# Performance work log

Hardware: AMD Instinct MI355X
Metric: run time of the kernel (lower is better)

## Reference

```python
import jax, jax.numpy as jnp
import numpy as np

N_WIRES = 16
VAR_DEPTH = 2
BATCH = 16


def _param_sizes():
    sizes = []
    n = N_WIRES
    lay = 0
    while n > 1:
        sizes.append(4 * int(np.ceil(N_WIRES / 2 ** lay)) * VAR_DEPTH)
        n = (n + 1) // 2
        lay += 1
    return sizes  # [128, 64, 32, 16]


def _apply_1q(psi, gate, w):
    # psi: (B, 2, ..., 2); gate: (2,2) complex; wire w lives on axis w+1
    psi = jnp.moveaxis(psi, w + 1, -1)
    psi = jnp.einsum('...j,ij->...i', psi, gate)
    return jnp.moveaxis(psi, -1, w + 1)


def _rx(psi, th, w):
    c = jnp.cos(th / 2).astype(jnp.complex64)
    s = jnp.sin(th / 2).astype(jnp.complex64)
    gate = jnp.stack([jnp.stack([c, -1j * s]), jnp.stack([-1j * s, c])])
    return _apply_1q(psi, gate, w)


def _rz(psi, th, w):
    ph = jnp.exp(0.5j * th * jnp.array([-1.0, 1.0], jnp.float32)).astype(jnp.complex64)
    shape = [1] * psi.ndim
    shape[w + 1] = 2
    return psi * ph.reshape(shape)


def _rzz(psi, th, wa, wb):
    # diag(e^{-i t/2}, e^{i t/2}, e^{i t/2}, e^{-i t/2}) -> sign = -1 if bits equal else +1
    sgn = jnp.array([[-1.0, 1.0], [1.0, -1.0]], jnp.float32)
    ph = jnp.exp(0.5j * th * sgn).astype(jnp.complex64)  # symmetric, transpose-safe
    a, b = min(wa, wb) + 1, max(wa, wb) + 1
    shape = [1] * psi.ndim
    shape[a] = 2
    shape[b] = 2
    return psi * ph.reshape(shape)


def _cnot(psi, c, t):
    p0 = jax.lax.slice_in_dim(psi, 0, 1, axis=c + 1)
    p1 = jax.lax.slice_in_dim(psi, 1, 2, axis=c + 1)
    return jnp.concatenate([p0, jnp.flip(p1, axis=t + 1)], axis=c + 1)


def _conv_layer(psi, params, active):
    n = len(active)
    for d in range(VAR_DEPTH):
        for j in range(n):
            base = 4 * j + d * 4 * n
            psi = _rx(psi, params[base + 0], active[j])
            psi = _rz(psi, params[base + 1], active[j])
            psi = _rx(psi, params[base + 2], active[j])
        for bg in (0, 1):
            for j in range(bg, n, 2):
                jn = (j + 1) % n  # ring coupling (wraps last->first)
                base = 4 * j + d * 4 * n
                psi = _rzz(psi, params[base + 3], active[j], active[jn])
    return psi


def _pool(psi, active):
    for j in range(0, len(active), 2):
        if j + 1 < len(active):
            psi = _cnot(psi, active[j], active[j + 1])
    return psi, active[::2]


def _forward(psi, params_list):
    active = list(range(N_WIRES))
    for p in params_list:
        psi = _conv_layer(psi, p, active)
        if len(active) > 1:
            psi, active = _pool(psi, active)
    w = active[0]  # measure Z on the surviving wire (wire 0)
    prob = psi.real ** 2 + psi.imag ** 2
    axes = tuple(a for a in range(1, psi.ndim) if a != w + 1)
    p2 = prob.sum(axis=axes)  # (B, 2)
    return p2[:, 0] - p2[:, 1]


def setup_inputs() -> dict:
    key = jax.random.key(0)
    ks = jax.random.split(key, 8)
    dim = 2 ** N_WIRES
    x_re = jax.random.normal(ks[0], (BATCH, dim), dtype=jnp.float32)
    x_im = jax.random.normal(ks[1], (BATCH, dim), dtype=jnp.float32)
    nrm = jnp.sqrt(jnp.sum(x_re ** 2 + x_im ** 2, axis=1, keepdims=True))
    x_re = x_re / nrm
    x_im = x_im / nrm
    sizes = _param_sizes()
    two_pi = 2.0 * np.pi
    params = [jax.random.uniform(ks[2 + i], (sizes[i],), dtype=jnp.float32) * two_pi
              for i in range(len(sizes))]
    return {"x_re": x_re, "x_im": x_im,
            "params0": params[0], "params1": params[1],
            "params2": params[2], "params3": params[3]}


def reference(x_re, x_im, params0, params1, params2, params3):
    psi = (x_re + 1j * x_im).astype(jnp.complex64)
    psi = psi.reshape((BATCH,) + (2,) * N_WIRES)
    return _forward(psi, [params0, params1, params2, params3])
```

## Files before the change

### kernel.cpp

```cpp
#include <hip/hip_runtime.h>


#define DEV __device__ __forceinline__
#define TB(i) (tbl + (i)*8)

__device__ static const unsigned char G_CP[60] = {
  15,14,13,12,11,10,9,8,7,6,5,4,3,2,1,0,
  15,14,13,12,11,10,9,8,7,6,5,4,3,2,1,0,
  15,13,11,9,7,5,3,1,
  15,13,11,9,7,5,3,1,
  15,11,7,3,
  15,11,7,3,
  15,7,
  15,7
};
__device__ static const unsigned char G_CQ[60] = {
  14,13,12,11,10,9,8,7,6,5,4,3,2,1,0,15,
  14,13,12,11,10,9,8,7,6,5,4,3,2,1,0,15,
  13,11,9,7,5,3,1,15,
  13,11,9,7,5,3,1,15,
  11,7,3,15,
  11,7,3,15,
  7,15,
  7,15
};

DEV float2 F2(float x, float y){ float2 r; r.x = x; r.y = y; return r; }
DEV float2 cmulf(float2 a, float2 b){ return F2(a.x*b.x - a.y*b.y, a.x*b.y + a.y*b.x); }
DEV int swz(int j){ return j ^ ((j>>4)&15) ^ ((j>>6)&15); }

template<int B>
DEV void gate8(float2* a, const float* __restrict__ g){
  float u00r=g[0],u00i=g[1],u01r=g[2],u01i=g[3],u10r=g[4],u10i=g[5],u11r=g[6],u11i=g[7];
  #pragma unroll
  for (int m=0; m<4; m++){
    int i0 = ((m>>B)<<(B+1)) | (m & ((1<<B)-1));
    int i1 = i0 | (1<<B);
    float2 x0=a[i0], x1=a[i1];
    a[i0] = F2(u00r*x0.x - u00i*x0.y + u01r*x1.x - u01i*x1.y,
               u00r*x0.y + u00i*x0.x + u01r*x1.y + u01i*x1.x);
    a[i1] = F2(u10r*x0.x - u10i*x0.y + u11r*x1.x - u11i*x1.y,
               u10r*x0.y + u10i*x0.x + u11r*x1.y + u11i*x1.x);
  }
}

template<int CB,int TB>
DEV void cnot8(float2* a){
  #pragma unroll
  for (int r=0; r<8; r++){
    if ( ((r>>CB)&1)==1 && ((r>>TB)&1)==0 ){
      float2 tmp = a[r]; a[r] = a[r | (1<<TB)]; a[r | (1<<TB)] = tmp;
    }
  }
}

template<int C0,int N,unsigned M0,unsigned M1,unsigned M2>
DEV void diag8(float2* a, const float* __restrict__ tbl, unsigned Ib){
  const unsigned regmask = M0|M1|M2;
  float2 F0 = F2(1.f, 0.f);
  #pragma unroll
  for (int k=0; k<N; k++){
    const int p = G_CP[C0+k], q = G_CQ[C0+k];
    if ( !(((1u<<p)|(1u<<q)) & regmask) ){
      float c = tbl[480 + 2*(C0+k)], s = tbl[481 + 2*(C0+k)];
      unsigned x = ((Ib>>p) ^ (Ib>>q)) & 1u;
      F0 = cmulf(F0, F2(c, x ? s : -s));
    }
  }
  #pragma unroll
  for (int r=0; r<8; r++){
    unsigned Ir = Ib ^ ((r&1)?M0:0u) ^ ((r&2)?M1:0u) ^ ((r&4)?M2:0u);
    float2 ph = F0;
    #pragma unroll
    for (int k=0; k<N; k++){
      const int p = G_CP[C0+k], q = G_CQ[C0+k];
      if ( ((1u<<p)|(1u<<q)) & regmask ){
        float c = tbl[480 + 2*(C0+k)], s = tbl[481 + 2*(C0+k)];
        unsigned x = ((Ir>>p) ^ (Ir>>q)) & 1u;
        ph = cmulf(ph, F2(c, x ? s : -s));
      }
    }
    a[r] = cmulf(a[r], ph);
  }
}

__global__ void k_setup(const float* __restrict__ p0, const float* __restrict__ p1,
                        const float* __restrict__ p2, const float* __restrict__ p3,
                        float* __restrict__ tbl, float* __restrict__ out){
  int g = threadIdx.x;
  if (g < 16) out[g] = 0.f;
  if (g >= 60) return;
  int d, j, n; const float* P;
  if (g < 32)      { n=16; d=(g>>4)&1; j=g&15; P=p0; }
  else if (g < 48) { n=8;  d=(g>>3)&1; j=g&7;  P=p1; }
  else if (g < 56) { n=4;  d=(g>>2)&1; j=g&3;  P=p2; }
  else             { n=2;  d=(g>>1)&1; j=g&1;  P=p3; }
  int base = 4*j + 4*n*d;
  double th0 = P[base+0], th1 = P[base+1], th2 = P[base+2], th3 = P[base+3];
  double c0 = cos(th0*0.5), s0 = sin(th0*0.5);
  double ca = cos(th1*0.5), sa = sin(th1*0.5);
  double c2 = cos(th2*0.5), s2 = sin(th2*0.5);
  double B00r =  ca*c0, B00i = -sa*c0;
  double B01r = -sa*s0, B01i = -ca*s0;
  double B10r =  sa*s0, B10i = -ca*s0;
  double B11r =  ca*c0, B11i =  sa*c0;
  double U00r = c2*B00r + s2*B10i, U00i = c2*B00i - s2*B10r;
  double U01r = c2*B01r + s2*B11i, U01i = c2*B01i - s2*B11r;
  double U10r = s2*B00i + c2*B10r, U10i = -s2*B00r + c2*B10i;
  double U11r = s2*B01i + c2*B11r, U11i = -s2*B01r + c2*B11i;
  float* o = tbl + g*8;
  o[0]=(float)U00r; o[1]=(float)U00i; o[2]=(float)U01r; o[3]=(float)U01i;
  o[4]=(float)U10r; o[5]=(float)U10i; o[6]=(float)U11r; o[7]=(float)U11i;
  tbl[480 + 2*g] = (float)cos(th3*0.5);
  tbl[481 + 2*g] = (float)sin(th3*0.5);
}

__global__ __launch_bounds__(128) void k_pass1(const float* __restrict__ xre, const float* __restrict__ xim,
                                               const float* __restrict__ tbl, float2* __restrict__ st){
  const int t = threadIdx.x;
  const int batch = blockIdx.x >> 6, o = blockIdx.x & 63;
  const unsigned hi = ((unsigned)batch<<16) | ((unsigned)o<<10);
  __shared__ float2 lds[2][1024];
  float2 a[8];
  {
    unsigned base = hi | ((unsigned)t<<3);
    float4 r0 = *(const float4*)(xre+base), r1 = *(const float4*)(xre+base+4);
    float4 i0 = *(const float4*)(xim+base), i1 = *(const float4*)(xim+base+4);
    a[0]=F2(r0.x,i0.x); a[1]=F2(r0.y,i0.y); a[2]=F2(r0.z,i0.z); a[3]=F2(r0.w,i0.w);
    a[4]=F2(r1.x,i1.x); a[5]=F2(r1.y,i1.y); a[6]=F2(r1.z,i1.z); a[7]=F2(r1.w,i1.w);
  }
  gate8<0>(a, TB(15)); gate8<1>(a, TB(14)); gate8<2>(a, TB(13));
  #pragma unroll
  for (int r=0;r<8;r++) lds[0][swz(r | (t<<3))] = a[r];
  __syncthreads();
  #pragma unroll
  for (int r=0;r<8;r++) a[r] = lds[0][swz((t&7) | (r<<3) | ((t>>3)<<6))];
  gate8<0>(a, TB(12)); gate8<1>(a, TB(11)); gate8<2>(a, TB(10));
  #pragma unroll
  for (int r=0;r<8;r++) lds[1][swz((t&7) | (r<<3) | ((t>>3)<<6))] = a[r];
  __syncthreads();
  #pragma unroll
  for (int r=0;r<8;r++) a[r] = lds[1][swz((t&63) | (r<<6) | ((t>>6)<<9))];
  gate8<0>(a, TB(9)); gate8<1>(a, TB(8)); gate8<2>(a, TB(7));
  #pragma unroll
  for (int r=0;r<8;r++) lds[0][swz((t&63) | (r<<6) | ((t>>6)<<9))] = a[r];
  __syncthreads();
  #pragma unroll
  for (int r=0;r<8;r++) a[r] = lds[0][swz(t | (r<<7))];
  gate8<2>(a, TB(6));
  #pragma unroll
  for (int r=0;r<8;r++) st[hi | (unsigned)(t | (r<<7))] = a[r];
}

DEV unsigned p2I(int j, int o){ return (unsigned)((j&15) | (o<<4) | ((j>>4)<<10)); }

__global__ __launch_bounds__(128) void k_pass2(const float* __restrict__ tbl, float2* __restrict__ st){
  const int t = threadIdx.x;
  const int batch = blockIdx.x >> 6, o = blockIdx.x & 63;
  const unsigned bb = (unsigned)batch<<16;
  __shared__ float2 lds[2][1024];
  float2 a[8];
  #pragma unroll
  for (int r=0;r<8;r++) a[r] = st[bb | p2I(t | (r<<7), o)];
  gate8<0>(a, TB(2)); gate8<1>(a, TB(1)); gate8<2>(a, TB(0));
  #pragma unroll
  for (int r=0;r<8;r++) lds[0][swz(t | (r<<7))] = a[r];
  __syncthreads();
  #pragma unroll
  for (int r=0;r<8;r++) a[r] = lds[0][swz((t&15) | (r<<4) | ((t>>4)<<7))];
  gate8<0>(a, TB(5)); gate8<1>(a, TB(4)); gate8<2>(a, TB(3));
  diag8<0,16, (1u<<10),(1u<<11),(1u<<12)>(a, tbl, p2I((t&15) | ((t>>4)<<7), o));
  gate8<0>(a, TB(21)); gate8<1>(a, TB(20)); gate8<2>(a, TB(19));
  #pragma unroll
  for (int r=0;r<8;r++) lds[1][swz((t&15) | (r<<4) | ((t>>4)<<7))] = a[r];
  __syncthreads();
  #pragma unroll
  for (int r=0;r<8;r++) a[r] = lds[1][swz(t | (r<<7))];
  gate8<0>(a, TB(18)); gate8<1>(a, TB(17)); gate8<2>(a, TB(16));
  #pragma unroll
  for (int r=0;r<8;r++) lds[0][swz(t | (r<<7))] = a[r];
  __syncthreads();
  #pragma unroll
  for (int r=0;r<8;r++) a[r] = lds[0][swz(r | (t<<3))];
  gate8<0>(a, TB(31)); gate8<1>(a, TB(30)); gate8<2>(a, TB(29));
  #pragma unroll
  for (int r=0;r<8;r++) lds[1][swz(r | (t<<3))] = a[r];
  __syncthreads();
  #pragma unroll
  for (int r=0;r<8;r++) a[r] = lds[1][swz((t&7) | (r<<3) | ((t>>3)<<6))];
  gate8<0>(a, TB(28));
  #pragma unroll
  for (int r=0;r<8;r++) st[bb | p2I((t&7) | (r<<3) | ((t>>3)<<6), o)] = a[r];
}

__global__ __launch_bounds__(128) void k_pass3(const float* __restrict__ tbl, float2* __restrict__ st){
  const int t = threadIdx.x;
  const int batch = blockIdx.x >> 6, o = blockIdx.x & 63;
  const unsigned hi = ((unsigned)batch<<16) | ((unsigned)o<<10);
  __shared__ float2 lds[2][1024];
  float2 a[8];
  #pragma unroll
  for (int r=0;r<8;r++) a[r] = st[hi | (unsigned)((t&15) | (r<<4) | ((t>>4)<<7))];
  gate8<0>(a, TB(27)); gate8<1>(a, TB(26)); gate8<2>(a, TB(25));
  #pragma unroll
  for (int r=0;r<8;r++) lds[0][swz((t&15) | (r<<4) | ((t>>4)<<7))] = a[r];
  __syncthreads();
  #pragma unroll
  for (int r=0;r<8;r++) a[r] = lds[0][swz(t | (r<<7))];
  gate8<0>(a, TB(24)); gate8<1>(a, TB(23)); gate8<2>(a, TB(22));
  diag8<16,16, (1u<<7),(1u<<8),(1u<<9)>(a, tbl, (unsigned)t | ((unsigned)o<<10));
  #pragma unroll
  for (int r=0;r<8;r++) st[hi | (unsigned)(t | (r<<7))] = a[r];
}

DEV unsigned p4I(int j, unsigned og){
  return (unsigned)( (j&15) | (((j>>4)&1)<<5) | (((j>>5)&1)<<7) | (((j>>6)&1)<<9)
                   | (((j>>7)&1)<<11) | (((j>>8)&1)<<13) | (((j>>9)&1)<<15) ) | og;
}
DEV int p4_jA(int t,int r){ return t | (r<<7); }
DEV int p4_jB(int t,int r){ return (t&15) | (r<<4) | ((t>>4)<<7); }
DEV int p4_jC(int t,int r){ return (t&1) | ((r&1)<<1) | (((t>>1)&1)<<2) | (((r>>1)&1)<<3)
                                  | (((t>>2)&1)<<4) | (((r>>2)&1)<<5) | ((t>>3)<<6); }
DEV int p4_jD(int t,int r){ return (t&15) | ((r&1)<<4) | (((t>>4)&1)<<5) | (((r>>1)&1)<<6)
                                  | (((t>>5)&1)<<7) | (((r>>2)&1)<<8) | ((t>>6)<<9); }
DEV int p4_jF(int t,int r){ return (t&63) | ((r&1)<<6) | (((r>>1)&1)<<7) | (((t>>6)&1)<<8) | ((r>>2)<<9); }
DEV int p4_jG(int t,int r){ return (t&15) | ((r&3)<<4) | (((t>>4)&7)<<6) | ((r>>2)<<9); }
DEV int p4_jJ(int t,int r){ return (t&7) | ((r&1)<<3) | (((t>>3)&1)<<4) | (((r>>1)&1)<<5)
                                  | (((t>>4)&7)<<6) | ((r>>2)<<9); }

__global__ __launch_bounds__(128) void k_pass4(const float* __restrict__ tbl, float2* __restrict__ st,
                                               float* __restrict__ out){
  const int t = threadIdx.x;
  const int batch = blockIdx.x >> 6, o = blockIdx.x & 63;
  const unsigned bb = (unsigned)batch<<16;
  const unsigned og = ((unsigned)(o&1)<<4) | ((unsigned)(o&2)<<5) | ((unsigned)(o&4)<<6)
                    | ((unsigned)(o&8)<<7) | ((unsigned)(o&16)<<8) | ((unsigned)(o&32)<<9);
  __shared__ float2 lds[2][1024];
  float2 a[8];
  #pragma unroll
  for (int r=0;r<8;r++){
    unsigned I = p4I(p4_jA(t,r), og);
    unsigned s1 = I ^ ((I & 0xAAAAu) >> 1);
    a[r] = st[bb | s1];
  }
  gate8<0>(a, TB(34)); gate8<1>(a, TB(33)); gate8<2>(a, TB(32));
  #pragma unroll
  for (int r=0;r<8;r++) lds[0][swz(p4_jA(t,r))] = a[r];
  __syncthreads();
  #pragma unroll
  for (int r=0;r<8;r++) a[r] = lds[0][swz(p4_jB(t,r))];
  gate8<0>(a, TB(37)); gate8<1>(a, TB(36)); gate8<2>(a, TB(35));
  #pragma unroll
  for (int r=0;r<8;r++) lds[1][swz(p4_jB(t,r))] = a[r];
  __syncthreads();
  #pragma unroll
  for (int r=0;r<8;r++) a[r] = lds[1][swz(p4_jC(t,r))];
  gate8<0>(a, TB(39)); gate8<1>(a, TB(38));
  diag8<32,8, 2u,8u,128u>(a, tbl, p4I(p4_jC(t,0), og));
  gate8<0>(a, TB(47)); gate8<1>(a, TB(46)); gate8<2>(a, TB(44));
  #pragma unroll
  for (int r=0;r<8;r++) lds[0][swz(p4_jC(t,r))] = a[r];
  __syncthreads();
  #pragma unroll
  for (int r=0;r<8;r++) a[r] = lds[0][swz(p4_jD(t,r))];
  gate8<0>(a, TB(45)); gate8<1>(a, TB(43)); gate8<2>(a, TB(41));
  #pragma unroll
  for (int r=0;r<8;r++) lds[1][swz(p4_jD(t,r))] = a[r];
  __syncthreads();
  #pragma unroll
  for (int r=0;r<8;r++) a[r] = lds[1][swz(p4_jA(t,r))];
  gate8<0>(a, TB(42)); gate8<2>(a, TB(40));
  diag8<40,8, (1u<<11),(1u<<13),(1u<<15)>(a, tbl, p4I(p4_jA(t,0), og));
  cnot8<2,1>(a);
  gate8<2>(a, TB(48));
  #pragma unroll
  for (int r=0;r<8;r++) lds[0][swz(p4_jA(t,r))] = a[r];
  __syncthreads();
  #pragma unroll
  for (int r=0;r<8;r++) a[r] = lds[0][swz(p4_jF(t,r))];
  cnot8<1,0>(a);
  gate8<1>(a, TB(49));
  #pragma unroll
  for (int r=0;r<8;r++) lds[1][swz(p4_jF(t,r))] = a[r];
  __syncthreads();
  #pragma unroll
  for (int r=0;r<8;r++) a[r] = lds[1][swz(p4_jG(t,r))];
  cnot8<1,0>(a);
  gate8<1>(a, TB(50));
  #pragma unroll
  for (int r=0;r<8;r++) lds[0][swz(p4_jG(t,r))] = a[r];
  __syncthreads();
  #pragma unroll
  for (int r=0;r<8;r++) a[r] = lds[0][swz(p4_jC(t,r))];
  cnot8<1,0>(a);
  gate8<1>(a, TB(51));
  diag8<48,4, 2u,8u,128u>(a, tbl, p4I(p4_jC(t,0), og));
  gate8<1>(a, TB(55)); gate8<2>(a, TB(54));
  #pragma unroll
  for (int r=0;r<8;r++) lds[1][swz(p4_jC(t,r))] = a[r];
  __syncthreads();
  #pragma unroll
  for (int r=0;r<8;r++) a[r] = lds[1][swz(p4_jA(t,r))];
  gate8<0>(a, TB(53)); gate8<2>(a, TB(52));
  diag8<52,4, (1u<<11),(1u<<13),(1u<<15)>(a, tbl, p4I(p4_jA(t,0), og));
  cnot8<2,0>(a);
  gate8<2>(a, TB(56));
  #pragma unroll
  for (int r=0;r<8;r++) lds[0][swz(p4_jA(t,r))] = a[r];
  __syncthreads();
  #pragma unroll
  for (int r=0;r<8;r++) a[r] = lds[0][swz(p4_jJ(t,r))];
  cnot8<1,0>(a);
  gate8<1>(a, TB(57));
  diag8<56,2, 8u,128u,(1u<<15)>(a, tbl, p4I(p4_jJ(t,0), og));
  gate8<2>(a, TB(58));
  float s = 0.f;
  #pragma unroll
  for (int r=0;r<8;r++){
    float w = a[r].x*a[r].x + a[r].y*a[r].y;
    s += (r & 4) ? -w : w;
  }
  #pragma unroll
  for (int off=32; off>0; off>>=1) s += __shfl_down(s, off);
  __syncthreads();
  float* red = reinterpret_cast<float*>(lds);
  if ((t & 63) == 0) red[t>>6] = s;
  __syncthreads();
  if (t == 0) atomicAdd(out + batch, red[0] + red[1]);
}

extern "C" void kernel_launch(void* const* d_in, const int* in_sizes, int n_in,
                              void* d_out, int out_size, void* d_ws, size_t ws_size,
                              hipStream_t stream) {
  const float* xre = (const float*)d_in[0];
  const float* xim = (const float*)d_in[1];
  const float* p0  = (const float*)d_in[2];
  const float* p1  = (const float*)d_in[3];
  const float* p2  = (const float*)d_in[4];
  const float* p3  = (const float*)d_in[5];
  float* out = (float*)d_out;
  float* tbl = (float*)d_ws;
  float2* st = (float2*)((char*)d_ws + 16384);

  k_setup<<<1, 64, 0, stream>>>(p0, p1, p2, p3, tbl, out);
  k_pass1<<<1024, 128, 0, stream>>>(xre, xim, tbl, st);
  k_pass2<<<1024, 128, 0, stream>>>(tbl, st);
  k_pass3<<<1024, 128, 0, stream>>>(tbl, st);
  k_pass4<<<1024, 128, 0, stream>>>(tbl, st, out);
}
```

Before: 122.8 us.

## Rewrite passes with 2048-amplitude tiles, 512 threads and 4 amplitudes per thread

Every pass kernel is rebuilt so that each block holds an 11-qubit tile of 2048 amplitudes in shared memory, using 512 threads that each keep 4 amplitudes and apply 2 gates between shuffles, replacing 128 threads holding 8 amplitudes each. The qubit-to-pass schedule, index maps, swizzle and the CNOT handling are redone, with CNOTs folded into register swaps and permuted shared-memory reads. The aim is more parallelism per block and fewer global round trips per qubit. In exchange there are many more shared-memory shuffles and barriers per gate, which could cost more than it saves.

After: 114.3 us. 1.07x faster.

```diff
diff --git a/kernel.cpp b/kernel.cpp
--- a/kernel.cpp
+++ b/kernel.cpp
@@ -2,7 +2,7 @@
 
 
 #define DEV __device__ __forceinline__
-#define TB(i) (tbl + (i)*8)
+#define TBL(i) (tbl + (i)*8)
 
 __device__ static const unsigned char G_CP[60] = {
   15,14,13,12,11,10,9,8,7,6,5,4,3,2,1,0,
@@ -27,15 +27,26 @@
 
 DEV float2 F2(float x, float y){ float2 r; r.x = x; r.y = y; return r; }
 DEV float2 cmulf(float2 a, float2 b){ return F2(a.x*b.x - a.y*b.y, a.x*b.y + a.y*b.x); }
-DEV int swz(int j){ return j ^ ((j>>4)&15) ^ ((j>>6)&15); }
-
-template<int B>
-DEV void gate8(float2* a, const float* __restrict__ g){
+DEV int swz(int j){ return j ^ ((j>>4)&15) ^ ((j>>8)&15); }
+
+template<int A,int B>
+DEV int mapj(int t, int s){
+  int j = ((s&1)<<A) | (((s>>1)&1)<<B);
+  int ti = 0;
+  #pragma unroll
+  for (int b=0;b<11;b++){
+    if (b!=A && b!=B){ j |= ((t>>ti)&1)<<b; ti++; }
+  }
+  return j;
+}
+
+template<int SB>
+DEV void gate4(float2* a, const float* __restrict__ g){
   float u00r=g[0],u00i=g[1],u01r=g[2],u01i=g[3],u10r=g[4],u10i=g[5],u11r=g[6],u11i=g[7];
   #pragma unroll
-  for (int m=0; m<4; m++){
-    int i0 = ((m>>B)<<(B+1)) | (m & ((1<<B)-1));
-    int i1 = i0 | (1<<B);
+  for (int m=0;m<2;m++){
+    int i0 = (SB==0) ? (m<<1) : m;
+    int i1 = i0 | (1<<SB);
     float2 x0=a[i0], x1=a[i1];
     a[i0] = F2(u00r*x0.x - u00i*x0.y + u01r*x1.x - u01i*x1.y,
                u00r*x0.y + u00i*x0.x + u01r*x1.y + u01i*x1.x);
@@ -44,22 +55,12 @@
   }
 }
 
-template<int CB,int TB>
-DEV void cnot8(float2* a){
-  #pragma unroll
-  for (int r=0; r<8; r++){
-    if ( ((r>>CB)&1)==1 && ((r>>TB)&1)==0 ){
-      float2 tmp = a[r]; a[r] = a[r | (1<<TB)]; a[r | (1<<TB)] = tmp;
-    }
-  }
-}
-
-template<int C0,int N,unsigned M0,unsigned M1,unsigned M2>
-DEV void diag8(float2* a, const float* __restrict__ tbl, unsigned Ib){
-  const unsigned regmask = M0|M1|M2;
+template<int C0,int N,unsigned M0,unsigned M1>
+DEV void diag4(float2* a, const float* __restrict__ tbl, unsigned Ib){
+  const unsigned regmask = M0|M1;
   float2 F0 = F2(1.f, 0.f);
   #pragma unroll
-  for (int k=0; k<N; k++){
+  for (int k=0;k<N;k++){
     const int p = G_CP[C0+k], q = G_CQ[C0+k];
     if ( !(((1u<<p)|(1u<<q)) & regmask) ){
       float c = tbl[480 + 2*(C0+k)], s = tbl[481 + 2*(C0+k)];
@@ -68,11 +69,11 @@
     }
   }
   #pragma unroll
-  for (int r=0; r<8; r++){
-    unsigned Ir = Ib ^ ((r&1)?M0:0u) ^ ((r&2)?M1:0u) ^ ((r&4)?M2:0u);
+  for (int r=0;r<4;r++){
+    unsigned Ir = Ib ^ ((r&1)?M0:0u) ^ ((r&2)?M1:0u);
     float2 ph = F0;
     #pragma unroll
-    for (int k=0; k<N; k++){
+    for (int k=0;k<N;k++){
       const int p = G_CP[C0+k], q = G_CQ[C0+k];
       if ( ((1u<<p)|(1u<<q)) & regmask ){
         float c = tbl[480 + 2*(C0+k)], s = tbl[481 + 2*(C0+k)];
@@ -83,6 +84,16 @@
     a[r] = cmulf(a[r], ph);
   }
 }
+
+DEV unsigned Ia(int j, int o){ return (unsigned)(j | (o<<11)); }
+DEV unsigned Ib2(int j, int o){ return (unsigned)((j&63) | (o<<6) | ((j>>6)<<11)); }
+DEV unsigned Ic(int j, int o){
+  return (unsigned)( ((j&1)<<1) | (((j>>1)&1)<<3) | (((j>>2)&1)<<5)
+       | (((j>>3)&63)<<6) | (((j>>9)&1)<<13) | (((j>>10)&1)<<15)
+       | (o&1) | (((o>>1)&1)<<2) | (((o>>2)&1)<<4) | (((o>>3)&1)<<12) | (((o>>4)&1)<<14) );
+}
+DEV int s2perm(int j){ return j ^ (((j>>8)&1)<<6) ^ (((j>>4)&1)<<2) ^ (((j>>1)&1)<<0); }
+DEV int s3perm(int j){ return j ^ (((j>>10)&1)<<8) ^ (((j>>4)&1)<<1); }
 
 __global__ void k_setup(const float* __restrict__ p0, const float* __restrict__ p1,
                         const float* __restrict__ p2, const float* __restrict__ p3,
@@ -104,229 +115,250 @@
   double B01r = -sa*s0, B01i = -ca*s0;
   double B10r =  sa*s0, B10i = -ca*s0;
   double B11r =  ca*c0, B11i =  sa*c0;
-  double U00r = c2*B00r + s2*B10i, U00i = c2*B00i - s2*B10r;
-  double U01r = c2*B01r + s2*B11i, U01i = c2*B01i - s2*B11r;
-  double U10r = s2*B00i + c2*B10r, U10i = -s2*B00r + c2*B10i;
-  double U11r = s2*B01i + c2*B11r, U11i = -s2*B01r + c2*B11i;
   float* o = tbl + g*8;
-  o[0]=(float)U00r; o[1]=(float)U00i; o[2]=(float)U01r; o[3]=(float)U01i;
-  o[4]=(float)U10r; o[5]=(float)U10i; o[6]=(float)U11r; o[7]=(float)U11i;
+  o[0]=(float)(c2*B00r + s2*B10i); o[1]=(float)(c2*B00i - s2*B10r);
+  o[2]=(float)(c2*B01r + s2*B11i); o[3]=(float)(c2*B01i - s2*B11r);
+  o[4]=(float)(s2*B00i + c2*B10r); o[5]=(float)(-s2*B00r + c2*B10i);
+  o[6]=(float)(s2*B01i + c2*B11r); o[7]=(float)(-s2*B01r + c2*B11i);
   tbl[480 + 2*g] = (float)cos(th3*0.5);
   tbl[481 + 2*g] = (float)sin(th3*0.5);
 }
 
-__global__ __launch_bounds__(128) void k_pass1(const float* __restrict__ xre, const float* __restrict__ xim,
-                                               const float* __restrict__ tbl, float2* __restrict__ st){
+__global__ __launch_bounds__(512, 4)
+void k_p1(const float* __restrict__ xre, const float* __restrict__ xim,
+          const float* __restrict__ tbl, float2* __restrict__ st){
   const int t = threadIdx.x;
-  const int batch = blockIdx.x >> 6, o = blockIdx.x & 63;
-  const unsigned hi = ((unsigned)batch<<16) | ((unsigned)o<<10);
-  __shared__ float2 lds[2][1024];
-  float2 a[8];
+  const int batch = blockIdx.x >> 5, o = blockIdx.x & 31;
+  const unsigned hi = ((unsigned)batch<<16) | ((unsigned)o<<11);
+  __shared__ float2 lds[2][2048];
+  float2 a[4];
   {
-    unsigned base = hi | ((unsigned)t<<3);
-    float4 r0 = *(const float4*)(xre+base), r1 = *(const float4*)(xre+base+4);
-    float4 i0 = *(const float4*)(xim+base), i1 = *(const float4*)(xim+base+4);
-    a[0]=F2(r0.x,i0.x); a[1]=F2(r0.y,i0.y); a[2]=F2(r0.z,i0.z); a[3]=F2(r0.w,i0.w);
-    a[4]=F2(r1.x,i1.x); a[5]=F2(r1.y,i1.y); a[6]=F2(r1.z,i1.z); a[7]=F2(r1.w,i1.w);
-  }
-  gate8<0>(a, TB(15)); gate8<1>(a, TB(14)); gate8<2>(a, TB(13));
-  #pragma unroll
-  for (int r=0;r<8;r++) lds[0][swz(r | (t<<3))] = a[r];
-  __syncthreads();
-  #pragma unroll
-  for (int r=0;r<8;r++) a[r] = lds[0][swz((t&7) | (r<<3) | ((t>>3)<<6))];
-  gate8<0>(a, TB(12)); gate8<1>(a, TB(11)); gate8<2>(a, TB(10));
-  #pragma unroll
-  for (int r=0;r<8;r++) lds[1][swz((t&7) | (r<<3) | ((t>>3)<<6))] = a[r];
-  __syncthreads();
-  #pragma unroll
-  for (int r=0;r<8;r++) a[r] = lds[1][swz((t&63) | (r<<6) | ((t>>6)<<9))];
-  gate8<0>(a, TB(9)); gate8<1>(a, TB(8)); gate8<2>(a, TB(7));
-  #pragma unroll
-  for (int r=0;r<8;r++) lds[0][swz((t&63) | (r<<6) | ((t>>6)<<9))] = a[r];
-  __syncthreads();
-  #pragma unroll
-  for (int r=0;r<8;r++) a[r] = lds[0][swz(t | (r<<7))];
-  gate8<2>(a, TB(6));
-  #pragma unroll
-  for (int r=0;r<8;r++) st[hi | (unsigned)(t | (r<<7))] = a[r];
-}
-
-DEV unsigned p2I(int j, int o){ return (unsigned)((j&15) | (o<<4) | ((j>>4)<<10)); }
-
-__global__ __launch_bounds__(128) void k_pass2(const float* __restrict__ tbl, float2* __restrict__ st){
+    unsigned base = hi | ((unsigned)t<<2);
+    float4 re = *(const float4*)(xre + base);
+    float4 im = *(const float4*)(xim + base);
+    a[0]=F2(re.x,im.x); a[1]=F2(re.y,im.y); a[2]=F2(re.z,im.z); a[3]=F2(re.w,im.w);
+  }
+  gate4<0>(a, TBL(15)); gate4<1>(a, TBL(14));
+  #pragma unroll
+  for (int s=0;s<4;s++) lds[0][swz(mapj<0,1>(t,s))] = a[s];
+  __syncthreads();
+  #pragma unroll
+  for (int s=0;s<4;s++) a[s] = lds[0][swz(mapj<2,3>(t,s))];
+  gate4<0>(a, TBL(13)); gate4<1>(a, TBL(12));
+  #pragma unroll
+  for (int s=0;s<4;s++) lds[1][swz(mapj<2,3>(t,s))] = a[s];
+  __syncthreads();
+  #pragma unroll
+  for (int s=0;s<4;s++) a[s] = lds[1][swz(mapj<4,5>(t,s))];
+  gate4<0>(a, TBL(11)); gate4<1>(a, TBL(10));
+  #pragma unroll
+  for (int s=0;s<4;s++) lds[0][swz(mapj<4,5>(t,s))] = a[s];
+  __syncthreads();
+  #pragma unroll
+  for (int s=0;s<4;s++) a[s] = lds[0][swz(mapj<6,7>(t,s))];
+  gate4<0>(a, TBL(9)); gate4<1>(a, TBL(8));
+  #pragma unroll
+  for (int s=0;s<4;s++) lds[1][swz(mapj<6,7>(t,s))] = a[s];
+  __syncthreads();
+  #pragma unroll
+  for (int s=0;s<4;s++) a[s] = lds[1][swz(mapj<8,9>(t,s))];
+  gate4<0>(a, TBL(7)); gate4<1>(a, TBL(6));
+  #pragma unroll
+  for (int s=0;s<4;s++) lds[0][swz(mapj<8,9>(t,s))] = a[s];
+  __syncthreads();
+  #pragma unroll
+  for (int s=0;s<4;s++) a[s] = lds[0][swz(mapj<0,10>(t,s))];
+  gate4<1>(a, TBL(5));
+  #pragma unroll
+  for (int s=0;s<4;s++) st[hi | (unsigned)mapj<0,10>(t,s)] = a[s];
+}
+
+__global__ __launch_bounds__(512, 4)
+void k_p2(const float* __restrict__ tbl, float2* __restrict__ st){
   const int t = threadIdx.x;
-  const int batch = blockIdx.x >> 6, o = blockIdx.x & 63;
+  const int batch = blockIdx.x >> 5, o = blockIdx.x & 31;
   const unsigned bb = (unsigned)batch<<16;
-  __shared__ float2 lds[2][1024];
-  float2 a[8];
-  #pragma unroll
-  for (int r=0;r<8;r++) a[r] = st[bb | p2I(t | (r<<7), o)];
-  gate8<0>(a, TB(2)); gate8<1>(a, TB(1)); gate8<2>(a, TB(0));
-  #pragma unroll
-  for (int r=0;r<8;r++) lds[0][swz(t | (r<<7))] = a[r];
-  __syncthreads();
-  #pragma unroll
-  for (int r=0;r<8;r++) a[r] = lds[0][swz((t&15) | (r<<4) | ((t>>4)<<7))];
-  gate8<0>(a, TB(5)); gate8<1>(a, TB(4)); gate8<2>(a, TB(3));
-  diag8<0,16, (1u<<10),(1u<<11),(1u<<12)>(a, tbl, p2I((t&15) | ((t>>4)<<7), o));
-  gate8<0>(a, TB(21)); gate8<1>(a, TB(20)); gate8<2>(a, TB(19));
-  #pragma unroll
-  for (int r=0;r<8;r++) lds[1][swz((t&15) | (r<<4) | ((t>>4)<<7))] = a[r];
-  __syncthreads();
-  #pragma unroll
-  for (int r=0;r<8;r++) a[r] = lds[1][swz(t | (r<<7))];
-  gate8<0>(a, TB(18)); gate8<1>(a, TB(17)); gate8<2>(a, TB(16));
-  #pragma unroll
-  for (int r=0;r<8;r++) lds[0][swz(t | (r<<7))] = a[r];
-  __syncthreads();
-  #pragma unroll
-  for (int r=0;r<8;r++) a[r] = lds[0][swz(r | (t<<3))];
-  gate8<0>(a, TB(31)); gate8<1>(a, TB(30)); gate8<2>(a, TB(29));
-  #pragma unroll
-  for (int r=0;r<8;r++) lds[1][swz(r | (t<<3))] = a[r];
-  __syncthreads();
-  #pragma unroll
-  for (int r=0;r<8;r++) a[r] = lds[1][swz((t&7) | (r<<3) | ((t>>3)<<6))];
-  gate8<0>(a, TB(28));
-  #pragma unroll
-  for (int r=0;r<8;r++) st[bb | p2I((t&7) | (r<<3) | ((t>>3)<<6), o)] = a[r];
-}
-
-__global__ __launch_bounds__(128) void k_pass3(const float* __restrict__ tbl, float2* __restrict__ st){
+  __shared__ float2 lds[2][2048];
+  float2 a[4];
+  #pragma unroll
+  for (int s=0;s<4;s++) a[s] = st[bb | Ib2(mapj<10,9>(t,s), o)];
+  gate4<0>(a, TBL(0)); gate4<1>(a, TBL(1));
+  #pragma unroll
+  for (int s=0;s<4;s++) lds[0][swz(mapj<10,9>(t,s))] = a[s];
+  __syncthreads();
+  #pragma unroll
+  for (int s=0;s<4;s++) a[s] = lds[0][swz(mapj<8,7>(t,s))];
+  gate4<0>(a, TBL(2)); gate4<1>(a, TBL(3));
+  #pragma unroll
+  for (int s=0;s<4;s++) lds[1][swz(mapj<8,7>(t,s))] = a[s];
+  __syncthreads();
+  #pragma unroll
+  for (int s=0;s<4;s++) a[s] = lds[1][swz(mapj<6,5>(t,s))];
+  gate4<0>(a, TBL(4));
+  diag4<0,16, (1u<<11),(1u<<5)>(a, tbl, Ib2(mapj<6,5>(t,0), o));
+  gate4<0>(a, TBL(20)); gate4<1>(a, TBL(26));
+  #pragma unroll
+  for (int s=0;s<4;s++) lds[0][swz(mapj<6,5>(t,s))] = a[s];
+  __syncthreads();
+  #pragma unroll
+  for (int s=0;s<4;s++) a[s] = lds[0][swz(mapj<7,8>(t,s))];
+  gate4<0>(a, TBL(19)); gate4<1>(a, TBL(18));
+  #pragma unroll
+  for (int s=0;s<4;s++) lds[1][swz(mapj<7,8>(t,s))] = a[s];
+  __syncthreads();
+  #pragma unroll
+  for (int s=0;s<4;s++) a[s] = lds[1][swz(mapj<9,10>(t,s))];
+  gate4<0>(a, TBL(17)); gate4<1>(a, TBL(16));
+  #pragma unroll
+  for (int s=0;s<4;s++) lds[0][swz(mapj<9,10>(t,s))] = a[s];
+  __syncthreads();
+  #pragma unroll
+  for (int s=0;s<4;s++) a[s] = lds[0][swz(mapj<0,1>(t,s))];
+  gate4<0>(a, TBL(31)); gate4<1>(a, TBL(30));
+  #pragma unroll
+  for (int s=0;s<4;s++) lds[1][swz(mapj<0,1>(t,s))] = a[s];
+  __syncthreads();
+  #pragma unroll
+  for (int s=0;s<4;s++) a[s] = lds[1][swz(mapj<2,3>(t,s))];
+  gate4<0>(a, TBL(29)); gate4<1>(a, TBL(28));
+  #pragma unroll
+  for (int s=0;s<4;s++) lds[0][swz(mapj<2,3>(t,s))] = a[s];
+  __syncthreads();
+  #pragma unroll
+  for (int s=0;s<4;s++) a[s] = lds[0][swz(mapj<4,10>(t,s))];
+  gate4<0>(a, TBL(27));
+  #pragma unroll
+  for (int s=0;s<4;s++) st[bb | Ib2(mapj<4,10>(t,s), o)] = a[s];
+}
+
+__global__ __launch_bounds__(512, 4)
+void k_p3(const float* __restrict__ tbl, float2* __restrict__ st){
   const int t = threadIdx.x;
-  const int batch = blockIdx.x >> 6, o = blockIdx.x & 63;
-  const unsigned hi = ((unsigned)batch<<16) | ((unsigned)o<<10);
-  __shared__ float2 lds[2][1024];
-  float2 a[8];
-  #pragma unroll
-  for (int r=0;r<8;r++) a[r] = st[hi | (unsigned)((t&15) | (r<<4) | ((t>>4)<<7))];
-  gate8<0>(a, TB(27)); gate8<1>(a, TB(26)); gate8<2>(a, TB(25));
-  #pragma unroll
-  for (int r=0;r<8;r++) lds[0][swz((t&15) | (r<<4) | ((t>>4)<<7))] = a[r];
-  __syncthreads();
-  #pragma unroll
-  for (int r=0;r<8;r++) a[r] = lds[0][swz(t | (r<<7))];
-  gate8<0>(a, TB(24)); gate8<1>(a, TB(23)); gate8<2>(a, TB(22));
-  diag8<16,16, (1u<<7),(1u<<8),(1u<<9)>(a, tbl, (unsigned)t | ((unsigned)o<<10));
-  #pragma unroll
-  for (int r=0;r<8;r++) st[hi | (unsigned)(t | (r<<7))] = a[r];
-}
-
-DEV unsigned p4I(int j, unsigned og){
-  return (unsigned)( (j&15) | (((j>>4)&1)<<5) | (((j>>5)&1)<<7) | (((j>>6)&1)<<9)
-                   | (((j>>7)&1)<<11) | (((j>>8)&1)<<13) | (((j>>9)&1)<<15) ) | og;
-}
-DEV int p4_jA(int t,int r){ return t | (r<<7); }
-DEV int p4_jB(int t,int r){ return (t&15) | (r<<4) | ((t>>4)<<7); }
-DEV int p4_jC(int t,int r){ return (t&1) | ((r&1)<<1) | (((t>>1)&1)<<2) | (((r>>1)&1)<<3)
-                                  | (((t>>2)&1)<<4) | (((r>>2)&1)<<5) | ((t>>3)<<6); }
-DEV int p4_jD(int t,int r){ return (t&15) | ((r&1)<<4) | (((t>>4)&1)<<5) | (((r>>1)&1)<<6)
-                                  | (((t>>5)&1)<<7) | (((r>>2)&1)<<8) | ((t>>6)<<9); }
-DEV int p4_jF(int t,int r){ return (t&63) | ((r&1)<<6) | (((r>>1)&1)<<7) | (((t>>6)&1)<<8) | ((r>>2)<<9); }
-DEV int p4_jG(int t,int r){ return (t&15) | ((r&3)<<4) | (((t>>4)&7)<<6) | ((r>>2)<<9); }
-DEV int p4_jJ(int t,int r){ return (t&7) | ((r&1)<<3) | (((t>>3)&1)<<4) | (((r>>1)&1)<<5)
-                                  | (((t>>4)&7)<<6) | ((r>>2)<<9); }
-
-__global__ __launch_bounds__(128) void k_pass4(const float* __restrict__ tbl, float2* __restrict__ st,
-                                               float* __restrict__ out){
+  const int batch = blockIdx.x >> 5, o = blockIdx.x & 31;
+  const unsigned hi = ((unsigned)batch<<16) | ((unsigned)o<<11);
+  __shared__ float2 lds[2][2048];
+  float2 a[4];
+  #pragma unroll
+  for (int s=0;s<4;s++) a[s] = st[hi | (unsigned)mapj<6,7>(t,s)];
+  gate4<0>(a, TBL(25)); gate4<1>(a, TBL(24));
+  #pragma unroll
+  for (int s=0;s<4;s++) lds[0][swz(mapj<6,7>(t,s))] = a[s];
+  __syncthreads();
+  #pragma unroll
+  for (int s=0;s<4;s++) a[s] = lds[0][swz(mapj<8,9>(t,s))];
+  gate4<0>(a, TBL(23)); gate4<1>(a, TBL(22));
+  #pragma unroll
+  for (int s=0;s<4;s++) lds[1][swz(mapj<8,9>(t,s))] = a[s];
+  __syncthreads();
+  #pragma unroll
+  for (int s=0;s<4;s++) a[s] = lds[1][swz(mapj<0,10>(t,s))];
+  gate4<1>(a, TBL(21));
+  diag4<16,16, 1u,(1u<<10)>(a, tbl, Ia(mapj<0,10>(t,0), o));
+  #pragma unroll
+  for (int s=0;s<4;s++) st[hi | (unsigned)mapj<0,10>(t,s)] = a[s];
+}
+
+__global__ __launch_bounds__(512, 4)
+void k_p4(const float* __restrict__ tbl, float2* __restrict__ st, float* __restrict__ out){
   const int t = threadIdx.x;
-  const int batch = blockIdx.x >> 6, o = blockIdx.x & 63;
+  const int batch = blockIdx.x >> 5, o = blockIdx.x & 31;
   const unsigned bb = (unsigned)batch<<16;
-  const unsigned og = ((unsigned)(o&1)<<4) | ((unsigned)(o&2)<<5) | ((unsigned)(o&4)<<6)
-                    | ((unsigned)(o&8)<<7) | ((unsigned)(o&16)<<8) | ((unsigned)(o&32)<<9);
-  __shared__ float2 lds[2][1024];
-  float2 a[8];
-  #pragma unroll
-  for (int r=0;r<8;r++){
-    unsigned I = p4I(p4_jA(t,r), og);
-    unsigned s1 = I ^ ((I & 0xAAAAu) >> 1);
-    a[r] = st[bb | s1];
-  }
-  gate8<0>(a, TB(34)); gate8<1>(a, TB(33)); gate8<2>(a, TB(32));
-  #pragma unroll
-  for (int r=0;r<8;r++) lds[0][swz(p4_jA(t,r))] = a[r];
-  __syncthreads();
-  #pragma unroll
-  for (int r=0;r<8;r++) a[r] = lds[0][swz(p4_jB(t,r))];
-  gate8<0>(a, TB(37)); gate8<1>(a, TB(36)); gate8<2>(a, TB(35));
-  #pragma unroll
-  for (int r=0;r<8;r++) lds[1][swz(p4_jB(t,r))] = a[r];
-  __syncthreads();
-  #pragma unroll
-  for (int r=0;r<8;r++) a[r] = lds[1][swz(p4_jC(t,r))];
-  gate8<0>(a, TB(39)); gate8<1>(a, TB(38));
-  diag8<32,8, 2u,8u,128u>(a, tbl, p4I(p4_jC(t,0), og));
-  gate8<0>(a, TB(47)); gate8<1>(a, TB(46)); gate8<2>(a, TB(44));
-  #pragma unroll
-  for (int r=0;r<8;r++) lds[0][swz(p4_jC(t,r))] = a[r];
-  __syncthreads();
-  #pragma unroll
-  for (int r=0;r<8;r++) a[r] = lds[0][swz(p4_jD(t,r))];
-  gate8<0>(a, TB(45)); gate8<1>(a, TB(43)); gate8<2>(a, TB(41));
-  #pragma unroll
-  for (int r=0;r<8;r++) lds[1][swz(p4_jD(t,r))] = a[r];
-  __syncthreads();
-  #pragma unroll
-  for (int r=0;r<8;r++) a[r] = lds[1][swz(p4_jA(t,r))];
-  gate8<0>(a, TB(42)); gate8<2>(a, TB(40));
-  diag8<40,8, (1u<<11),(1u<<13),(1u<<15)>(a, tbl, p4I(p4_jA(t,0), og));
-  cnot8<2,1>(a);
-  gate8<2>(a, TB(48));
-  #pragma unroll
-  for (int r=0;r<8;r++) lds[0][swz(p4_jA(t,r))] = a[r];
-  __syncthreads();
-  #pragma unroll
-  for (int r=0;r<8;r++) a[r] = lds[0][swz(p4_jF(t,r))];
-  cnot8<1,0>(a);
-  gate8<1>(a, TB(49));
-  #pragma unroll
-  for (int r=0;r<8;r++) lds[1][swz(p4_jF(t,r))] = a[r];
-  __syncthreads();
-  #pragma unroll
-  for (int r=0;r<8;r++) a[r] = lds[1][swz(p4_jG(t,r))];
-  cnot8<1,0>(a);
-  gate8<1>(a, TB(50));
-  #pragma unroll
-  for (int r=0;r<8;r++) lds[0][swz(p4_jG(t,r))] = a[r];
-  __syncthreads();
-  #pragma unroll
-  for (int r=0;r<8;r++) a[r] = lds[0][swz(p4_jC(t,r))];
-  cnot8<1,0>(a);
-  gate8<1>(a, TB(51));
-  diag8<48,4, 2u,8u,128u>(a, tbl, p4I(p4_jC(t,0), og));
-  gate8<1>(a, TB(55)); gate8<2>(a, TB(54));
-  #pragma unroll
-  for (int r=0;r<8;r++) lds[1][swz(p4_jC(t,r))] = a[r];
-  __syncthreads();
-  #pragma unroll
-  for (int r=0;r<8;r++) a[r] = lds[1][swz(p4_jA(t,r))];
-  gate8<0>(a, TB(53)); gate8<2>(a, TB(52));
-  diag8<52,4, (1u<<11),(1u<<13),(1u<<15)>(a, tbl, p4I(p4_jA(t,0), og));
-  cnot8<2,0>(a);
-  gate8<2>(a, TB(56));
-  #pragma unroll
-  for (int r=0;r<8;r++) lds[0][swz(p4_jA(t,r))] = a[r];
-  __syncthreads();
-  #pragma unroll
-  for (int r=0;r<8;r++) a[r] = lds[0][swz(p4_jJ(t,r))];
-  cnot8<1,0>(a);
-  gate8<1>(a, TB(57));
-  diag8<56,2, 8u,128u,(1u<<15)>(a, tbl, p4I(p4_jJ(t,0), og));
-  gate8<2>(a, TB(58));
+  __shared__ float2 lds[2][2048];
+  __shared__ float red[8];
+  float2 a[4];
+  #pragma unroll
+  for (int s=0;s<4;s++){
+    unsigned I = Ic(mapj<10,9>(t,s), o);
+    I ^= (I & 0xAAAAu) >> 1;
+    a[s] = st[bb | I];
+  }
+  gate4<0>(a, TBL(32)); gate4<1>(a, TBL(33));
+  #pragma unroll
+  for (int s=0;s<4;s++) lds[0][swz(mapj<10,9>(t,s))] = a[s];
+  __syncthreads();
+  #pragma unroll
+  for (int s=0;s<4;s++) a[s] = lds[0][swz(mapj<8,6>(t,s))];
+  gate4<0>(a, TBL(34)); gate4<1>(a, TBL(35));
+  #pragma unroll
+  for (int s=0;s<4;s++) lds[1][swz(mapj<8,6>(t,s))] = a[s];
+  __syncthreads();
+  #pragma unroll
+  for (int s=0;s<4;s++) a[s] = lds[1][swz(mapj<4,2>(t,s))];
+  gate4<0>(a, TBL(36)); gate4<1>(a, TBL(37));
+  #pragma unroll
+  for (int s=0;s<4;s++) lds[0][swz(mapj<4,2>(t,s))] = a[s];
+  __syncthreads();
+  #pragma unroll
+  for (int s=0;s<4;s++) a[s] = lds[0][swz(mapj<1,0>(t,s))];
+  gate4<0>(a, TBL(38)); gate4<1>(a, TBL(39));
+  diag4<32,8, (1u<<3),(1u<<1)>(a, tbl, Ic(mapj<1,0>(t,0), o));
+  gate4<0>(a, TBL(46)); gate4<1>(a, TBL(47));
+  #pragma unroll
+  for (int s=0;s<4;s++) lds[1][swz(mapj<1,0>(t,s))] = a[s];
+  __syncthreads();
+  #pragma unroll
+  for (int s=0;s<4;s++) a[s] = lds[1][swz(mapj<2,4>(t,s))];
+  gate4<0>(a, TBL(45)); gate4<1>(a, TBL(44));
+  #pragma unroll
+  for (int s=0;s<4;s++) lds[0][swz(mapj<2,4>(t,s))] = a[s];
+  __syncthreads();
+  #pragma unroll
+  for (int s=0;s<4;s++) a[s] = lds[0][swz(mapj<6,8>(t,s))];
+  gate4<0>(a, TBL(43)); gate4<1>(a, TBL(42));
+  #pragma unroll
+  for (int s=0;s<4;s++) lds[1][swz(mapj<6,8>(t,s))] = a[s];
+  __syncthreads();
+  #pragma unroll
+  for (int s=0;s<4;s++) a[s] = lds[1][swz(mapj<9,10>(t,s))];
+  gate4<0>(a, TBL(41)); gate4<1>(a, TBL(40));
+  diag4<40,8, (1u<<13),(1u<<15)>(a, tbl, Ic(mapj<9,10>(t,0), o));
+  { float2 tmp=a[2]; a[2]=a[3]; a[3]=tmp; }
+  gate4<1>(a, TBL(48));
+  #pragma unroll
+  for (int s=0;s<4;s++) lds[0][swz(mapj<9,10>(t,s))] = a[s];
+  __syncthreads();
+  #pragma unroll
+  for (int s=0;s<4;s++) a[s] = lds[0][swz(s2perm(mapj<8,4>(t,s)))];
+  gate4<0>(a, TBL(49)); gate4<1>(a, TBL(50));
+  #pragma unroll
+  for (int s=0;s<4;s++) lds[1][swz(mapj<8,4>(t,s))] = a[s];
+  __syncthreads();
+  #pragma unroll
+  for (int s=0;s<4;s++) a[s] = lds[1][swz(mapj<1,10>(t,s))];
+  gate4<0>(a, TBL(51));
+  diag4<48,4, (1u<<3),(1u<<15)>(a, tbl, Ic(mapj<1,10>(t,0), o));
+  gate4<0>(a, TBL(55)); gate4<1>(a, TBL(52));
+  #pragma unroll
+  for (int s=0;s<4;s++) lds[0][swz(mapj<1,10>(t,s))] = a[s];
+  __syncthreads();
+  #pragma unroll
+  for (int s=0;s<4;s++) a[s] = lds[0][swz(mapj<4,8>(t,s))];
+  gate4<0>(a, TBL(54)); gate4<1>(a, TBL(53));
+  diag4<52,4, (1u<<7),(1u<<11)>(a, tbl, Ic(mapj<4,8>(t,0), o));
+  #pragma unroll
+  for (int s=0;s<4;s++) lds[1][swz(mapj<4,8>(t,s))] = a[s];
+  __syncthreads();
+  #pragma unroll
+  for (int s=0;s<4;s++) a[s] = lds[1][swz(s3perm(mapj<4,10>(t,s)))];
+  gate4<0>(a, TBL(57)); gate4<1>(a, TBL(56));
+  diag4<56,2, (1u<<7),(1u<<15)>(a, tbl, Ic(mapj<4,10>(t,0), o));
+  gate4<1>(a, TBL(58));
   float s = 0.f;
   #pragma unroll
-  for (int r=0;r<8;r++){
+  for (int r=0;r<4;r++){
     float w = a[r].x*a[r].x + a[r].y*a[r].y;
-    s += (r & 4) ? -w : w;
+    s += (r & 2) ? -w : w;
   }
   #pragma unroll
   for (int off=32; off>0; off>>=1) s += __shfl_down(s, off);
-  __syncthreads();
-  float* red = reinterpret_cast<float*>(lds);
   if ((t & 63) == 0) red[t>>6] = s;
   __syncthreads();
-  if (t == 0) atomicAdd(out + batch, red[0] + red[1]);
+  if (t == 0){
+    float tot = 0.f;
+    #pragma unroll
+    for (int w=0; w<8; w++) tot += red[w];
+    atomicAdd(out + batch, tot);
+  }
 }
 
 extern "C" void kernel_launch(void* const* d_in, const int* in_sizes, int n_in,
@@ -339,12 +371,12 @@
   const float* p2  = (const float*)d_in[4];
   const float* p3  = (const float*)d_in[5];
   float* out = (float*)d_out;
-  float* tbl = (float*)d_ws;
-  float2* st = (float2*)((char*)d_ws + 16384);
+  float2* st = (float2*)d_ws;
+  float* tbl = (float*)((char*)d_ws + (8u<<20));
 
   k_setup<<<1, 64, 0, stream>>>(p0, p1, p2, p3, tbl, out);
-  k_pass1<<<1024, 128, 0, stream>>>(xre, xim, tbl, st);
-  k_pass2<<<1024, 128, 0, stream>>>(tbl, st);
-  k_pass3<<<1024, 128, 0, stream>>>(tbl, st);
-  k_pass4<<<1024, 128, 0, stream>>>(tbl, st, out);
-}
+  k_p1<<<512, 512, 0, stream>>>(xre, xim, tbl, st);
+  k_p2<<<512, 512, 0, stream>>>(tbl, st);
+  k_p3<<<512, 512, 0, stream>>>(tbl, st);
+  k_p4<<<512, 512, 0, stream>>>(tbl, st, out);
+}
```
